# Optimization experiments

Measured on AMD Instinct MI355X. Metric: run time of the kernel, lower is better.

Reference implementation:

```python
import jax, jax.numpy as jnp
import numpy as np

N = 50000      # nodes
E = 800000     # edges
FIN = 128      # num_feature
EDIM = 16      # edge_dim
OUT = 64       # out_dim (per-head channels; concat=False averages heads)
H = 4          # heads
SCALE = 1.0 / float(np.sqrt(OUT))


def _layernorm(h, g, b):
    mu = h.mean(-1, keepdims=True)
    var = ((h - mu) ** 2).mean(-1, keepdims=True)
    return (h - mu) * jax.lax.rsqrt(var + 1e-5) * g + b


def _tconv(x, src, dst, ea, Wq, bq, Wk, bk, Wv, bv, We, Ws, bs):
    # PyG TransformerConv, concat=False, root_weight=True, eval mode (no dropout)
    n = x.shape[0]
    q = (x @ Wq + bq).reshape(n, H, OUT)[dst]   # [E,H,D] query at destination
    k = (x @ Wk + bk).reshape(n, H, OUT)[src]   # [E,H,D] key at source
    v = (x @ Wv + bv).reshape(n, H, OUT)[src]   # [E,H,D] value at source
    e = (ea @ We).reshape(-1, H, OUT)           # [E,H,D] edge embedding (no bias)
    logits = jnp.einsum('ehd,ehd->eh', q, k + e) * SCALE   # [E,H]
    # segment softmax over incoming edges of each destination node
    m = jax.lax.stop_gradient(jax.ops.segment_max(logits, dst, num_segments=n))
    a = jnp.exp(logits - m[dst])
    s = jax.ops.segment_sum(a, dst, num_segments=n)
    alpha = a / s[dst]                                     # [E,H]
    agg = jax.ops.segment_sum((v + e) * alpha[..., None], dst, num_segments=n)  # [N,H,D]
    return agg.mean(axis=1) + x @ Ws + bs      # concat=False -> head mean; + skip


def _forward(x, src, dst, ea, p1, p2, p3, g, b):
    h = x
    for p in (p1, p2, p3):
        h = jax.nn.gelu(_layernorm(_tconv(h, src, dst, ea, *p), g, b), approximate=False)
    return h


def setup_inputs() -> dict:
    key = jax.random.key(0)
    ks = iter(jax.random.split(key, 64))
    def nrm(shp, s=0.05):
        return jax.random.normal(next(ks), shp, jnp.float32) * s
    inp = {
        'x': nrm((N, FIN), 1.0),
        'edge_index': jax.random.randint(next(ks), (2, E), 0, N),
        'edge_attr': nrm((E, EDIM), 1.0),
    }
    for l, fin in ((1, FIN), (2, OUT), (3, OUT)):
        inp[f'Wq{l}'] = nrm((fin, H * OUT)); inp[f'bq{l}'] = jnp.zeros((H * OUT,), jnp.float32)
        inp[f'Wk{l}'] = nrm((fin, H * OUT)); inp[f'bk{l}'] = jnp.zeros((H * OUT,), jnp.float32)
        inp[f'Wv{l}'] = nrm((fin, H * OUT)); inp[f'bv{l}'] = jnp.zeros((H * OUT,), jnp.float32)
        inp[f'We{l}'] = nrm((EDIM, H * OUT))
        inp[f'Ws{l}'] = nrm((fin, OUT)); inp[f'bs{l}'] = jnp.zeros((OUT,), jnp.float32)
    inp['ln_g'] = jnp.ones((OUT,), jnp.float32)
    inp['ln_b'] = jnp.zeros((OUT,), jnp.float32)
    return inp


def reference(x, edge_index, edge_attr,
              Wq1, bq1, Wk1, bk1, Wv1, bv1, We1, Ws1, bs1,
              Wq2, bq2, Wk2, bk2, Wv2, bv2, We2, Ws2, bs2,
              Wq3, bq3, Wk3, bk3, Wv3, bv3, We3, Ws3, bs3,
              ln_g, ln_b):
    src, dst = edge_index[0], edge_index[1]
    p1 = (Wq1, bq1, Wk1, bk1, Wv1, bv1, We1, Ws1, bs1)
    p2 = (Wq2, bq2, Wk2, bk2, Wv2, bv2, We2, Ws2, bs2)
    p3 = (Wq3, bq3, Wk3, bk3, Wv3, bv3, We3, Ws3, bs3)
    return _forward(x, src, dst, edge_attr, p1, p2, p3, ln_g, ln_b)
```

## Files before the change

kernel.cpp:

```cpp
#include <hip/hip_runtime.h>
#include <hip/hip_bf16.h>
#include <math.h>

#define NNODES 50000
#define NEDGES 800000
#define HD     256
#define CW     384
#define NTOT   896
#define QS     0.18033688011112042f

typedef __hip_bfloat16 bf16;
typedef unsigned short u16;
typedef unsigned char  u8;
typedef unsigned int   u32;
typedef __attribute__((ext_vector_type(8))) short bf16x8;
typedef __attribute__((ext_vector_type(4))) float f32x4;
typedef __attribute__((ext_vector_type(2))) float f32x2;

__device__ __forceinline__ float lo16f(u32 u) { return __uint_as_float(u << 16); }
__device__ __forceinline__ float hi16f(u32 u) { return __uint_as_float(u & 0xFFFF0000u); }
__device__ __forceinline__ short f2s(float v) { __hip_bfloat16 h = __float2bfloat16(v); return *(short*)&h; }

template<int CTRL>
__device__ __forceinline__ float dppadd(float x) {
    int t = __builtin_amdgcn_update_dpp(0, __float_as_int(x), CTRL, 0xF, 0xF, true);
    return x + __int_as_float(t);
}

__global__ void hist_kernel(const int* __restrict__ dst, int* __restrict__ deg, int E) {
    int e = blockIdx.x * 256 + threadIdx.x;
    if (e < E) atomicAdd(&deg[dst[e]], 1);
}

__global__ void scanA(const int* __restrict__ deg, int* __restrict__ locincl,
                      int* __restrict__ blocksum, int n) {
    int tid = threadIdx.x;
    int i = blockIdx.x * 256 + tid;
    int v = (i < n) ? deg[i] : 0;
    int lane = tid & 63, w = tid >> 6;
    int s = v;
    #pragma unroll
    for (int off = 1; off < 64; off <<= 1) {
        int t = __shfl_up(s, off);
        if (lane >= off) s += t;
    }
    __shared__ int wsum[4];
    if (lane == 63) wsum[w] = s;
    __syncthreads();
    for (int ww = 0; ww < w; ww++) s += wsum[ww];
    if (i < n) locincl[i] = s;
    if (tid == 255) blocksum[blockIdx.x] = s;
}

__global__ void scanB(const int* __restrict__ blocksum, int* __restrict__ blockoff,
                      int nb, int* __restrict__ rowptr, int n) {
    int tid = threadIdx.x;
    int v = (tid < nb) ? blocksum[tid] : 0;
    int lane = tid & 63, w = tid >> 6;
    int s = v;
    #pragma unroll
    for (int off = 1; off < 64; off <<= 1) {
        int t = __shfl_up(s, off);
        if (lane >= off) s += t;
    }
    __shared__ int wsum[4];
    if (lane == 63) wsum[w] = s;
    __syncthreads();
    for (int ww = 0; ww < w; ww++) s += wsum[ww];
    if (tid < nb) blockoff[tid] = s - v;
    if (tid == 255) rowptr[n] = s;
}

__global__ void scanC(const int* __restrict__ deg, const int* __restrict__ locincl,
                      const int* __restrict__ blockoff,
                      int* __restrict__ rowptr, int* __restrict__ cursor, int n) {
    int i = blockIdx.x * 256 + threadIdx.x;
    if (i < n) {
        int ex = locincl[i] - deg[i] + blockoff[blockIdx.x];
        rowptr[i] = ex;
        cursor[i] = ex;
    }
}

__global__ void scatter_kernel(const int* __restrict__ src, const int* __restrict__ dst,
                               int* __restrict__ cursor, int2* __restrict__ csr2, int E) {
    int e = blockIdx.x * 256 + threadIdx.x;
    if (e < E) {
        int d = dst[e];
        int p = atomicAdd(&cursor[d], 1);
        csr2[p] = make_int2(src[e], e);
    }
}

__global__ void xcast(const float* __restrict__ x, u16* __restrict__ xb) {
    int i = blockIdx.x * 256 + threadIdx.x;
    const float4* p = (const float4*)(x + (size_t)i * 8);
    float4 a = p[0], b = p[1];
    union { u16 s[8]; uint4 u; } t;
    t.s[0] = (u16)f2s(a.x); t.s[1] = (u16)f2s(a.y); t.s[2] = (u16)f2s(a.z); t.s[3] = (u16)f2s(a.w);
    t.s[4] = (u16)f2s(b.x); t.s[5] = (u16)f2s(b.y); t.s[6] = (u16)f2s(b.z); t.s[7] = (u16)f2s(b.w);
    *(uint4*)(xb + (size_t)i * 8) = t.u;
}

__global__ void pack_all(const float* __restrict__ Wq, const float* __restrict__ bq,
                         const float* __restrict__ Wk, const float* __restrict__ bk,
                         const float* __restrict__ Wv, const float* __restrict__ bv,
                         const float* __restrict__ We,
                         const float* __restrict__ Ws, const float* __restrict__ bs,
                         bf16* __restrict__ Wc, float* __restrict__ b, int K) {
    int n = blockIdx.x, c = threadIdx.x;
    float v, bb;
    if (n < 256)      { v = Wq[(size_t)c * 256 + n] * QS;    bb = bq[n] * QS; }
    else if (n < 320) {
        int t = n - 256, h = t >> 4, j = t & 15;
        float s = 0.f, sb = 0.f;
        #pragma unroll 8
        for (int d = 0; d < 64; d++) {
            float wv = We[j * HD + h * 64 + d];
            s += Wq[(size_t)c * 256 + h * 64 + d] * wv;
            sb += bq[h * 64 + d] * wv;
        }
        v = s * QS; bb = sb * QS;
    }
    else if (n < 384) { v = Ws[(size_t)c * 64  + (n - 320)]; bb = bs[n - 320]; }
    else if (n < 640) { v = Wv[(size_t)c * 256 + (n - 384)]; bb = bv[n - 384]; }
    else              { v = Wk[(size_t)c * 256 + (n - 640)]; bb = bk[n - 640]; }
    Wc[(size_t)n * K + c] = __float2bfloat16(v);
    if (c == 0) b[n] = bb;
}

template<int K>
__global__ void __launch_bounds__(256) gemm_reg(
    const u16* __restrict__ A, const bf16* __restrict__ Wc, const float* __restrict__ bias,
    bf16* __restrict__ comb, bf16* __restrict__ vbuf, u8* __restrict__ k8)
{
    constexpr int KS = K / 32;
    constexpr int ITERS = 8;
    int tid = threadIdx.x, w = tid >> 6, lane = tid & 63;
    int cl = lane & 15, aq = lane >> 4;
    int chunk = blockIdx.x;
    int mrow = blockIdx.y * (64 * ITERS) + w * 16 + cl;

    bf16x8 bfr[4][KS];
    #pragma unroll
    for (int t = 0; t < 4; t++)
        #pragma unroll
        for (int ks = 0; ks < KS; ks++)
            bfr[t][ks] = *(const bf16x8*)((const u16*)Wc +
                         (size_t)(chunk * 64 + t * 16 + cl) * K + ks * 32 + aq * 8);

    float4 bv[4];
    #pragma unroll
    for (int t = 0; t < 4; t++) bv[t] = *(const float4*)&bias[chunk * 64 + t * 16 + aq * 4];

    auto LOADA = [&](bf16x8* af, int m) {
        int rc = (m < NNODES) ? m : (NNODES - 1);
        const u16* ar = A + (size_t)rc * K + aq * 8;
        #pragma unroll
        for (int ks = 0; ks < KS; ks++) af[ks] = *(const bf16x8*)(ar + ks * 32);
    };

    bf16x8 cur[KS], nxt[KS];
    LOADA(cur, mrow);
    #pragma unroll
    for (int it = 0; it < ITERS; it++) {
        int m = mrow + it * 64;
        if (it + 1 < ITERS) LOADA(nxt, m + 64);
        f32x4 acc[4] = {};
        #pragma unroll
        for (int t = 0; t < 4; t++)
            #pragma unroll
            for (int ks = 0; ks < KS; ks++)
                acc[t] = __builtin_amdgcn_mfma_f32_16x16x32_bf16(bfr[t][ks], cur[ks], acc[t], 0, 0, 0);

        if (m < NNODES) {
            if (chunk < 10) {
                u16* dst = (chunk < 6) ? (u16*)comb + (size_t)m * CW + chunk * 64
                                       : (u16*)vbuf + (size_t)m * 256 + (chunk - 6) * 64;
                #pragma unroll
                for (int t = 0; t < 4; t++) {
                    u32 lo = (u32)(u16)f2s(acc[t][0] + bv[t].x) | ((u32)(u16)f2s(acc[t][1] + bv[t].y) << 16);
                    u32 hi = (u32)(u16)f2s(acc[t][2] + bv[t].z) | ((u32)(u16)f2s(acc[t][3] + bv[t].w) << 16);
                    *(uint2*)(dst + t * 16 + aq * 4) = make_uint2(lo, hi);
                }
            } else {
                u8* dst = k8 + (size_t)m * 256 + (chunk - 10) * 64;
                #pragma unroll
                for (int t = 0; t < 4; t++) {
                    u32 pk = __builtin_amdgcn_cvt_pk_fp8_f32(acc[t][0] + bv[t].x, acc[t][1] + bv[t].y, 0, false);
                    pk = __builtin_amdgcn_cvt_pk_fp8_f32(acc[t][2] + bv[t].z, acc[t][3] + bv[t].w, pk, true);
                    *(u32*)(dst + t * 16 + aq * 4) = pk;
                }
            }
        }
        #pragma unroll
        for (int ks = 0; ks < KS; ks++) cur[ks] = nxt[ks];
    }
}

__global__ void __launch_bounds__(256) node_fused(
    const int* __restrict__ rowptr, const int2* __restrict__ csr2,
    const float* __restrict__ eattr, const u16* __restrict__ comb,
    const u16* __restrict__ vbuf, const u8* __restrict__ k8,
    const float* __restrict__ We, const float* __restrict__ lng, const float* __restrict__ lnb,
    bf16* __restrict__ outB, float* __restrict__ outF)
{
    int tid = threadIdx.x, w = tid >> 6, lane = tid & 63;
    int n = blockIdx.x * 2 + (w >> 1);
    int half = w & 1;
    int hg = lane >> 4, j16 = lane & 15, coff = 4 * lane;
    __shared__ float sAV[4][256];
    __shared__ float sAE[4][64];
    __shared__ float sSS[4][4];

    const u16* crow = comb + (size_t)n * CW;
    uint2 qv = *(const uint2*)(crow + coff);
    float qf0 = lo16f(qv.x), qf1 = hi16f(qv.x), qf2 = lo16f(qv.y), qf3 = hi16f(qv.y);
    float qwe_r = __uint_as_float((u32)crow[256 + lane] << 16);

    int e0 = __builtin_amdgcn_readfirstlane(rowptr[n]);
    int e1 = __builtin_amdgcn_readfirstlane(rowptr[n + 1]);
    int mid = e0 + ((e1 - e0 + 1) >> 1);
    int lo = half ? mid : e0;
    int hi = half ? e1 : mid;

    float ss = 0.f, av0 = 0.f, av1 = 0.f, av2 = 0.f, av3 = 0.f, ae = 0.f;
    u32 vo = (u32)coff * 2u;
    u32 eo = (u32)j16 * 4u;

    auto EDGE = [&](int2 me) {
        u32 s   = (u32)__builtin_amdgcn_readfirstlane(me.x);
        u32 eid = (u32)__builtin_amdgcn_readfirstlane(me.y);
        const char* kp = (const char*)k8    + ((size_t)s << 8);
        const char* vp = (const char*)vbuf  + ((size_t)s << 9);
        const char* ep = (const char*)eattr + ((size_t)eid << 6);
        u32   kw = *(const u32*)  (kp + coff);
        uint2 vw = *(const uint2*)(vp + vo);
        float ea = *(const float*)(ep + eo);
        f32x2 k01 = __builtin_amdgcn_cvt_pk_f32_fp8(kw, false);
        f32x2 k23 = __builtin_amdgcn_cvt_pk_f32_fp8(kw, true);
        float part = qf0 * k01[0] + qf1 * k01[1] + qf2 * k23[0] + qf3 * k23[1] + qwe_r * ea;
        part = dppadd<0xB1>(part);
        part = dppadd<0x4E>(part);
        part = dppadd<0x141>(part);
        part = dppadd<0x140>(part);
        float alpha = __builtin_amdgcn_exp2f(part);
        ss += alpha;
        ae += alpha * ea;
        av0 += alpha * lo16f(vw.x); av1 += alpha * hi16f(vw.x);
        av2 += alpha * lo16f(vw.y); av3 += alpha * hi16f(vw.y);
    };

    int i = lo;
    int2 c0 = make_int2(0, 0), c1 = c0, c2 = c0, c3 = c0;
    if (i + 3 < hi) { c0 = csr2[i]; c1 = csr2[i + 1]; c2 = csr2[i + 2]; c3 = csr2[i + 3]; }
    for (; i + 7 < hi; i += 4) {
        int2 p0 = csr2[i + 4], p1 = csr2[i + 5], p2 = csr2[i + 6], p3 = csr2[i + 7];
        EDGE(c0); EDGE(c1); EDGE(c2); EDGE(c3);
        c0 = p0; c1 = p1; c2 = p2; c3 = p3;
    }
    if (i + 3 < hi) { EDGE(c0); EDGE(c1); EDGE(c2); EDGE(c3); i += 4; }
    for (; i < hi; ++i) { int2 cc = csr2[i]; EDGE(cc); }

    *(float4*)&sAV[w][coff] = make_float4(av0, av1, av2, av3);
    sAE[w][lane] = ae;
    if (j16 == 0) sSS[w][hg] = ss;
    __syncthreads();

    if ((w & 1) == 0) {
        float inv[4];
        #pragma unroll
        for (int h = 0; h < 4; h++) {
            float S = sSS[w][h] + sSS[w + 1][h];
            inv[h] = (S > 0.f) ? 1.f / S : 0.f;
        }
        {
            float aet = (sAE[w][lane] + sAE[w + 1][lane]) * inv[hg];
            sAE[w][lane] = aet;
        }
        int d = lane;
        float val = 0.f;
        #pragma unroll
        for (int h = 0; h < 4; h++) {
            float AV = sAV[w][h * 64 + d] + sAV[w + 1][h * 64 + d];
            float xv = AV * inv[h];
            #pragma unroll
            for (int j = 0; j < 16; j++) xv += sAE[w][h * 16 + j] * We[j * HD + h * 64 + d];
            val += xv;
        }
        val = val * 0.25f + __uint_as_float((u32)crow[320 + d] << 16);

        float m = val;
        #pragma unroll
        for (int off = 1; off < 64; off <<= 1) m += __shfl_xor(m, off);
        m *= (1.f / 64.f);
        float diff = val - m;
        float vr = diff * diff;
        #pragma unroll
        for (int off = 1; off < 64; off <<= 1) vr += __shfl_xor(vr, off);
        vr *= (1.f / 64.f);
        float y = diff * rsqrtf(vr + 1e-5f) * lng[d] + lnb[d];
        float ge = 0.5f * y * (1.f + erff(y * 0.70710678118654752f));
        if (outF) outF[(size_t)n * 64 + d] = ge;
        else      outB[(size_t)n * 64 + d] = __float2bfloat16(ge);
    }
}

extern "C" void kernel_launch(void* const* d_in, const int* in_sizes, int n_in,
                              void* d_out, int out_size, void* d_ws, size_t ws_size,
                              hipStream_t stream)
{
    const float* x     = (const float*)d_in[0];
    const int*   eidx  = (const int*)d_in[1];
    const float* eattr = (const float*)d_in[2];
    struct P { const float *Wq,*bq,*Wk,*bk,*Wv,*bv,*We,*Ws,*bs; };
    P p[3];
    for (int l = 0; l < 3; l++) {
        int base = 3 + l * 9;
        p[l].Wq = (const float*)d_in[base + 0]; p[l].bq = (const float*)d_in[base + 1];
        p[l].Wk = (const float*)d_in[base + 2]; p[l].bk = (const float*)d_in[base + 3];
        p[l].Wv = (const float*)d_in[base + 4]; p[l].bv = (const float*)d_in[base + 5];
        p[l].We = (const float*)d_in[base + 6];
        p[l].Ws = (const float*)d_in[base + 7]; p[l].bs = (const float*)d_in[base + 8];
    }
    const float* lng = (const float*)d_in[30];
    const float* lnb = (const float*)d_in[31];

    char* ws = (char*)d_ws;
    size_t off = 0;
    auto alloc = [&](size_t bytes) { void* pp = ws + off; off += (bytes + 255) & ~(size_t)255; return pp; };
    int*   rowptr   = (int*)  alloc((NNODES + 1) * 4);
    int*   cursor   = (int*)  alloc(NNODES * 4);
    int*   deg      = (int*)  alloc(NNODES * 4);
    int*   blocksum = (int*)  alloc(256 * 4);
    int*   blockoff = (int*)  alloc(256 * 4);
    int2*  csr2     = (int2*) alloc((size_t)NEDGES * 8);
    bf16*  hbuf     = (bf16*) alloc((size_t)NNODES * 64 * 2);
    u16*   xb       = (u16*)  alloc((size_t)NNODES * 128 * 2);
    bf16*  comb     = (bf16*) alloc((size_t)NNODES * CW * 2);
    bf16*  vbuf     = (bf16*) alloc((size_t)NNODES * 256 * 2);
    u8*    k8       = (u8*)   alloc((size_t)NNODES * 256);
    bf16*  Wc       = (bf16*) alloc((size_t)NTOT * 128 * 2);
    float* b896     = (float*)alloc(NTOT * 4);
    (void)ws_size;

    const int* srcArr = eidx;
    const int* dstArr = eidx + NEDGES;

    int NB = (NNODES + 255) / 256;
    (void)hipMemsetAsync(deg, 0, NNODES * 4, stream);
    hist_kernel<<<(NEDGES + 255) / 256, 256, 0, stream>>>(dstArr, deg, NEDGES);
    scanA<<<NB, 256, 0, stream>>>(deg, cursor, blocksum, NNODES);
    scanB<<<1, 256, 0, stream>>>(blocksum, blockoff, NB, rowptr, NNODES);
    scanC<<<NB, 256, 0, stream>>>(deg, cursor, blockoff, rowptr, cursor, NNODES);
    scatter_kernel<<<(NEDGES + 255) / 256, 256, 0, stream>>>(srcArr, dstArr, cursor, csr2, NEDGES);
    xcast<<<(NNODES * 128 / 8 + 255) / 256, 256, 0, stream>>>(x, xb);

    int NBY = (NNODES + 511) / 512;
    int fins[3] = {128, 64, 64};

    const u16* hin = xb;
    for (int l = 0; l < 3; l++) {
        int FIN = fins[l];
        pack_all<<<NTOT, FIN, 0, stream>>>(p[l].Wq, p[l].bq, p[l].Wk, p[l].bk,
                                           p[l].Wv, p[l].bv, p[l].We, p[l].Ws, p[l].bs,
                                           Wc, b896, FIN);
        if (l == 0) gemm_reg<128><<<dim3(14, NBY), 256, 0, stream>>>(hin, Wc, b896, comb, vbuf, k8);
        else        gemm_reg<64> <<<dim3(14, NBY), 256, 0, stream>>>(hin, Wc, b896, comb, vbuf, k8);
        node_fused<<<NNODES / 2, 256, 0, stream>>>(rowptr, csr2, eattr, (const u16*)comb,
            (const u16*)vbuf, k8, p[l].We, lng, lnb,
            (l == 2) ? nullptr : hbuf, (l == 2) ? (float*)d_out : nullptr);
        hin = (const u16*)hbuf;
    }
}
```

Before: 763.8 us.

## Stage GEMM epilogue through LDS for coalesced stores; one wave per node in aggregation

The GEMM epilogue now writes each wave's 16-row tile into a per-wave shared-memory buffer and re-reads it as 16-byte row-contiguous chunks, so global stores are coalesced instead of scattered 8/4-byte writes. The A-operand prefetch is deepened from one to two iterations ahead. The node aggregation kernel drops the two-waves-per-node edge split and its block-wide sync, giving each wave a whole node and normalising locally, with four nodes per block. This trades intra-node parallelism and more registers for fewer barriers, less LDS traffic and better store efficiency. The LDS re-read in both kernels relies on wave-local ordering without an explicit barrier.

```diff
diff --git a/kernel.cpp b/kernel.cpp
--- a/kernel.cpp
+++ b/kernel.cpp
@@ -136,10 +136,13 @@
 {
     constexpr int KS = K / 32;
     constexpr int ITERS = 8;
+    __shared__ u8 TrB[4][2560];
     int tid = threadIdx.x, w = tid >> 6, lane = tid & 63;
     int cl = lane & 15, aq = lane >> 4;
     int chunk = blockIdx.x;
-    int mrow = blockIdx.y * (64 * ITERS) + w * 16 + cl;
+    int slab = blockIdx.y * (64 * ITERS);
+    int mrow = slab + w * 16 + cl;
+    u8* myT = TrB[w];
 
     bf16x8 bfr[4][KS];
     #pragma unroll
@@ -160,41 +163,55 @@
         for (int ks = 0; ks < KS; ks++) af[ks] = *(const bf16x8*)(ar + ks * 32);
     };
 
-    bf16x8 cur[KS], nxt[KS];
-    LOADA(cur, mrow);
+    bf16x8 b0[KS], b1[KS], b2[KS];
+    LOADA(b0, mrow);
+    LOADA(b1, mrow + 64);
     #pragma unroll
     for (int it = 0; it < ITERS; it++) {
         int m = mrow + it * 64;
-        if (it + 1 < ITERS) LOADA(nxt, m + 64);
+        if (it + 2 < ITERS) LOADA(b2, m + 128);
         f32x4 acc[4] = {};
         #pragma unroll
         for (int t = 0; t < 4; t++)
             #pragma unroll
             for (int ks = 0; ks < KS; ks++)
-                acc[t] = __builtin_amdgcn_mfma_f32_16x16x32_bf16(bfr[t][ks], cur[ks], acc[t], 0, 0, 0);
-
-        if (m < NNODES) {
-            if (chunk < 10) {
-                u16* dst = (chunk < 6) ? (u16*)comb + (size_t)m * CW + chunk * 64
-                                       : (u16*)vbuf + (size_t)m * 256 + (chunk - 6) * 64;
-                #pragma unroll
-                for (int t = 0; t < 4; t++) {
-                    u32 lo = (u32)(u16)f2s(acc[t][0] + bv[t].x) | ((u32)(u16)f2s(acc[t][1] + bv[t].y) << 16);
-                    u32 hi = (u32)(u16)f2s(acc[t][2] + bv[t].z) | ((u32)(u16)f2s(acc[t][3] + bv[t].w) << 16);
-                    *(uint2*)(dst + t * 16 + aq * 4) = make_uint2(lo, hi);
-                }
-            } else {
-                u8* dst = k8 + (size_t)m * 256 + (chunk - 10) * 64;
-                #pragma unroll
-                for (int t = 0; t < 4; t++) {
-                    u32 pk = __builtin_amdgcn_cvt_pk_fp8_f32(acc[t][0] + bv[t].x, acc[t][1] + bv[t].y, 0, false);
-                    pk = __builtin_amdgcn_cvt_pk_fp8_f32(acc[t][2] + bv[t].z, acc[t][3] + bv[t].w, pk, true);
-                    *(u32*)(dst + t * 16 + aq * 4) = pk;
+                acc[t] = __builtin_amdgcn_mfma_f32_16x16x32_bf16(bfr[t][ks], b0[ks], acc[t], 0, 0, 0);
+
+        if (chunk < 10) {
+            #pragma unroll
+            for (int t = 0; t < 4; t++) {
+                u32 lo = (u32)(u16)f2s(acc[t][0] + bv[t].x) | ((u32)(u16)f2s(acc[t][1] + bv[t].y) << 16);
+                u32 hi = (u32)(u16)f2s(acc[t][2] + bv[t].z) | ((u32)(u16)f2s(acc[t][3] + bv[t].w) << 16);
+                *(uint2*)(myT + cl * 160 + t * 32 + aq * 8) = make_uint2(lo, hi);
+            }
+            #pragma unroll
+            for (int i = 0; i < 2; i++) {
+                int r = i * 8 + (lane >> 3);
+                uint4 vv = *(const uint4*)(myT + r * 160 + (lane & 7) * 16);
+                int gr = slab + it * 64 + w * 16 + r;
+                if (gr < NNODES) {
+                    u16* dst = (chunk < 6) ? (u16*)comb + (size_t)gr * CW + chunk * 64
+                                           : (u16*)vbuf + (size_t)gr * 256 + (chunk - 6) * 64;
+                    *(uint4*)(dst + (lane & 7) * 8) = vv;
                 }
             }
+        } else {
+            #pragma unroll
+            for (int t = 0; t < 4; t++) {
+                u32 pk = __builtin_amdgcn_cvt_pk_fp8_f32(acc[t][0] + bv[t].x, acc[t][1] + bv[t].y, 0, false);
+                pk = __builtin_amdgcn_cvt_pk_fp8_f32(acc[t][2] + bv[t].z, acc[t][3] + bv[t].w, pk, true);
+                *(u32*)(myT + cl * 80 + (t * 4 + aq) * 4) = pk;
+            }
+            {
+                int r = lane >> 2;
+                uint4 vv = *(const uint4*)(myT + r * 80 + (lane & 3) * 16);
+                int gr = slab + it * 64 + w * 16 + r;
+                if (gr < NNODES)
+                    *(uint4*)(k8 + (size_t)gr * 256 + (chunk - 10) * 64 + (lane & 3) * 16) = vv;
+            }
         }
         #pragma unroll
-        for (int ks = 0; ks < KS; ks++) cur[ks] = nxt[ks];
+        for (int ks = 0; ks < KS; ks++) { b0[ks] = b1[ks]; b1[ks] = b2[ks]; }
     }
 }
 
@@ -206,12 +223,10 @@
     bf16* __restrict__ outB, float* __restrict__ outF)
 {
     int tid = threadIdx.x, w = tid >> 6, lane = tid & 63;
-    int n = blockIdx.x * 2 + (w >> 1);
-    int half = w & 1;
+    int n = blockIdx.x * 4 + w;
     int hg = lane >> 4, j16 = lane & 15, coff = 4 * lane;
     __shared__ float sAV[4][256];
     __shared__ float sAE[4][64];
-    __shared__ float sSS[4][4];
 
     const u16* crow = comb + (size_t)n * CW;
     uint2 qv = *(const uint2*)(crow + coff);
@@ -220,9 +235,6 @@
 
     int e0 = __builtin_amdgcn_readfirstlane(rowptr[n]);
     int e1 = __builtin_amdgcn_readfirstlane(rowptr[n + 1]);
-    int mid = e0 + ((e1 - e0 + 1) >> 1);
-    int lo = half ? mid : e0;
-    int hi = half ? e1 : mid;
 
     float ss = 0.f, av0 = 0.f, av1 = 0.f, av2 = 0.f, av3 = 0.f, ae = 0.f;
     u32 vo = (u32)coff * 2u;
@@ -251,59 +263,45 @@
         av2 += alpha * lo16f(vw.y); av3 += alpha * hi16f(vw.y);
     };
 
-    int i = lo;
+    int i = e0;
     int2 c0 = make_int2(0, 0), c1 = c0, c2 = c0, c3 = c0;
-    if (i + 3 < hi) { c0 = csr2[i]; c1 = csr2[i + 1]; c2 = csr2[i + 2]; c3 = csr2[i + 3]; }
-    for (; i + 7 < hi; i += 4) {
+    if (i + 3 < e1) { c0 = csr2[i]; c1 = csr2[i + 1]; c2 = csr2[i + 2]; c3 = csr2[i + 3]; }
+    for (; i + 7 < e1; i += 4) {
         int2 p0 = csr2[i + 4], p1 = csr2[i + 5], p2 = csr2[i + 6], p3 = csr2[i + 7];
         EDGE(c0); EDGE(c1); EDGE(c2); EDGE(c3);
         c0 = p0; c1 = p1; c2 = p2; c3 = p3;
     }
-    if (i + 3 < hi) { EDGE(c0); EDGE(c1); EDGE(c2); EDGE(c3); i += 4; }
-    for (; i < hi; ++i) { int2 cc = csr2[i]; EDGE(cc); }
-
-    *(float4*)&sAV[w][coff] = make_float4(av0, av1, av2, av3);
-    sAE[w][lane] = ae;
-    if (j16 == 0) sSS[w][hg] = ss;
-    __syncthreads();
-
-    if ((w & 1) == 0) {
-        float inv[4];
-        #pragma unroll
-        for (int h = 0; h < 4; h++) {
-            float S = sSS[w][h] + sSS[w + 1][h];
-            inv[h] = (S > 0.f) ? 1.f / S : 0.f;
-        }
-        {
-            float aet = (sAE[w][lane] + sAE[w + 1][lane]) * inv[hg];
-            sAE[w][lane] = aet;
-        }
-        int d = lane;
-        float val = 0.f;
-        #pragma unroll
-        for (int h = 0; h < 4; h++) {
-            float AV = sAV[w][h * 64 + d] + sAV[w + 1][h * 64 + d];
-            float xv = AV * inv[h];
-            #pragma unroll
-            for (int j = 0; j < 16; j++) xv += sAE[w][h * 16 + j] * We[j * HD + h * 64 + d];
-            val += xv;
-        }
-        val = val * 0.25f + __uint_as_float((u32)crow[320 + d] << 16);
-
-        float m = val;
-        #pragma unroll
-        for (int off = 1; off < 64; off <<= 1) m += __shfl_xor(m, off);
-        m *= (1.f / 64.f);
-        float diff = val - m;
-        float vr = diff * diff;
-        #pragma unroll
-        for (int off = 1; off < 64; off <<= 1) vr += __shfl_xor(vr, off);
-        vr *= (1.f / 64.f);
-        float y = diff * rsqrtf(vr + 1e-5f) * lng[d] + lnb[d];
-        float ge = 0.5f * y * (1.f + erff(y * 0.70710678118654752f));
-        if (outF) outF[(size_t)n * 64 + d] = ge;
-        else      outB[(size_t)n * 64 + d] = __float2bfloat16(ge);
-    }
+    if (i + 3 < e1) { EDGE(c0); EDGE(c1); EDGE(c2); EDGE(c3); i += 4; }
+    for (; i < e1; ++i) { int2 cc = csr2[i]; EDGE(cc); }
+
+    float inv = (ss > 0.f) ? 1.f / ss : 0.f;
+    *(float4*)&sAV[w][coff] = make_float4(av0 * inv, av1 * inv, av2 * inv, av3 * inv);
+    sAE[w][lane] = ae * inv;
+
+    int d = lane;
+    float val = 0.f;
+    #pragma unroll
+    for (int h = 0; h < 4; h++) {
+        float xv = sAV[w][h * 64 + d];
+        #pragma unroll
+        for (int j = 0; j < 16; j++) xv += sAE[w][h * 16 + j] * We[j * HD + h * 64 + d];
+        val += xv;
+    }
+    val = val * 0.25f + __uint_as_float((u32)crow[320 + d] << 16);
+
+    float m = val;
+    #pragma unroll
+    for (int off = 1; off < 64; off <<= 1) m += __shfl_xor(m, off);
+    m *= (1.f / 64.f);
+    float diff = val - m;
+    float vr = diff * diff;
+    #pragma unroll
+    for (int off = 1; off < 64; off <<= 1) vr += __shfl_xor(vr, off);
+    vr *= (1.f / 64.f);
+    float y = diff * rsqrtf(vr + 1e-5f) * lng[d] + lnb[d];
+    float ge = 0.5f * y * (1.f + erff(y * 0.70710678118654752f));
+    if (outF) outF[(size_t)n * 64 + d] = ge;
+    else      outB[(size_t)n * 64 + d] = __float2bfloat16(ge);
 }
 
 extern "C" void kernel_launch(void* const* d_in, const int* in_sizes, int n_in,
@@ -367,7 +365,7 @@
                                            Wc, b896, FIN);
         if (l == 0) gemm_reg<128><<<dim3(14, NBY), 256, 0, stream>>>(hin, Wc, b896, comb, vbuf, k8);
         else        gemm_reg<64> <<<dim3(14, NBY), 256, 0, stream>>>(hin, Wc, b896, comb, vbuf, k8);
-        node_fused<<<NNODES / 2, 256, 0, stream>>>(rowptr, csr2, eattr, (const u16*)comb,
+        node_fused<<<NNODES / 4, 256, 0, stream>>>(rowptr, csr2, eattr, (const u16*)comb,
             (const u16*)vbuf, k8, p[l].We, lng, lnb,
             (l == 2) ? nullptr : hbuf, (l == 2) ? (float*)d_out : nullptr);
         hin = (const u16*)hbuf;
```

Result: faster. 655.2 us (-14.2%).
